# Performance work log

Hardware: AMD Instinct MI355X
Metric: run time of the kernel (lower is better)

## Reference

```python
import jax, jax.numpy as jnp
import numpy as np

DIM = 1536; NH = 12; HD = 128; C2 = HD // 2          # rope half-dim = 64
F, H, W = 1, 30, 52
FRAME = H * W                                         # 1560 tokens/frame
SINK_FRAMES = 1; LOCAL_ATTN = 6
SINK = SINK_FRAMES * FRAME                            # 1560
MAX_ATTN = LOCAL_ATTN * 1560                          # 9360
CACHE = 9360                                          # kv cache length
GLOBAL_END = 9360; LOCAL_END_CACHE = 9360             # cache state before step
SPLITS = (C2 - 2 * (C2 // 3), C2 // 3, C2 // 3)       # (22, 21, 21)
EPS = 1e-6


def setup_inputs() -> dict:
    key = jax.random.key(0)
    ks = jax.random.split(key, 12)
    s = F * H * W
    rn = lambda k, sh, sc=1.0: jax.random.normal(k, sh, jnp.float32) * sc
    x = rn(ks[0], (1, s, DIM))
    Wq = rn(ks[1], (DIM, DIM), 0.02); Wk = rn(ks[2], (DIM, DIM), 0.02)
    Wv = rn(ks[3], (DIM, DIM), 0.02); Wo = rn(ks[4], (DIM, DIM), 0.02)
    zb = jnp.zeros((DIM,), jnp.float32)
    angles = jax.random.uniform(ks[5], (1024, C2), jnp.float32) * (2.0 * np.pi)
    freqs_cos = jnp.cos(angles); freqs_sin = jnp.sin(angles)
    cache_k = rn(ks[6], (1, CACHE, NH, HD)); cache_v = rn(ks[7], (1, CACHE, NH, HD))
    return dict(x=x, Wq=Wq, bq=zb, Wk=Wk, bk=zb, Wv=Wv, bv=zb, Wo=Wo, bo=zb,
                nq_w=jnp.ones((DIM,), jnp.float32), nk_w=jnp.ones((DIM,), jnp.float32),
                cache_k=cache_k, cache_v=cache_v,
                freqs_cos=freqs_cos, freqs_sin=freqs_sin,
                seq_lens=jnp.array([s], jnp.int32),
                grid_sizes=jnp.array([[F, H, W]], jnp.int32),
                current_start=GLOBAL_END)


def _rmsnorm(x, w):
    return x * jax.lax.rsqrt(jnp.mean(x * x, -1, keepdims=True) + EPS) * w


def _grid_table(table, start_frame):
    """table [1024, C2] -> per-token rope factors [S, 1, C2] over the (F,H,W) grid."""
    s0, s1, s2 = SPLITS
    tf, th, tw = table[:, :s0], table[:, s0:s0 + s1], table[:, s0 + s1:]
    fp = jnp.broadcast_to(tf[start_frame:start_frame + F][:, None, None, :], (F, H, W, s0))
    hp = jnp.broadcast_to(th[:H][None, :, None, :], (F, H, W, s1))
    wp = jnp.broadcast_to(tw[:W][None, None, :, :], (F, H, W, s2))
    return jnp.concatenate([fp, hp, wp], -1).reshape(F * H * W, 1, C2)


def _rope(x, cos, sin):
    # x: [b, s, n, d]; cos/sin: [s, 1, C2] (complex multiply in real arithmetic)
    b, s, n, d = x.shape
    xp = x.reshape(b, s, n, d // 2, 2)
    xr, xi = xp[..., 0], xp[..., 1]
    c, sn = cos[None], sin[None]                      # [1, s, 1, C2]
    out_r = xr * c - xi * sn
    out_i = xr * sn + xi * c
    return jnp.stack([out_r, out_i], -1).reshape(b, s, n, d)


def reference(x, Wq, bq, Wk, bk, Wv, bv, Wo, bo, nq_w, nk_w,
              cache_k, cache_v, freqs_cos, freqs_sin,
              seq_lens, grid_sizes, current_start):
    b, s = x.shape[:2]
    q = _rmsnorm(x @ Wq.T + bq, nq_w).reshape(b, s, NH, HD)
    k = _rmsnorm(x @ Wk.T + bk, nk_w).reshape(b, s, NH, HD)
    v = (x @ Wv.T + bv).reshape(b, s, NH, HD)

    start_frame = int(current_start) // FRAME
    cos = _grid_table(freqs_cos, start_frame)
    sin = _grid_table(freqs_sin, start_frame)
    rq = _rope(q, cos, sin)
    rk = _rope(k, cos, sin)

    # --- static cache bookkeeping (roll_and_insert path; all Python ints) ---
    num_new = s
    current_end = int(current_start) + num_new
    num_evicted = num_new + LOCAL_END_CACHE - CACHE           # 1560
    num_rolled = LOCAL_END_CACHE - num_evicted - SINK         # 6240
    local_end = LOCAL_END_CACHE + current_end - GLOBAL_END - num_evicted  # 9360
    local_start = local_end - num_new                         # 7800 == SINK + num_rolled
    temp_k = jnp.concatenate(
        [cache_k[:, :SINK], cache_k[:, SINK + num_evicted:SINK + num_evicted + num_rolled], rk], axis=1)
    temp_v = jnp.concatenate(
        [cache_v[:, :SINK], cache_v[:, SINK + num_evicted:SINK + num_evicted + num_rolled], v], axis=1)

    # --- sink + sliding-window attention ---
    local_budget = MAX_ATTN - SINK
    win_start = max(SINK, local_end - local_budget)
    k_cat = jnp.concatenate([temp_k[:, :SINK], temp_k[:, win_start:local_end]], axis=1)
    v_cat = jnp.concatenate([temp_v[:, :SINK], temp_v[:, win_start:local_end]], axis=1)

    logits = jnp.einsum('bqhd,bkhd->bhqk', rq, k_cat) * (HD ** -0.5)
    probs = jax.nn.softmax(logits, axis=-1)
    out = jnp.einsum('bhqk,bkhd->bqhd', probs, v_cat)
    y = out.reshape(b, s, DIM) @ Wo.T + bo
    return y
```

## Files before the change

### kernel.cpp

```cpp
#include <hip/hip_runtime.h>
#include <hip/hip_bf16.h>

typedef __bf16 bf16;
typedef __bf16 bf16x2 __attribute__((ext_vector_type(2)));
typedef __bf16 bf16x4 __attribute__((ext_vector_type(4)));
typedef __bf16 bf16x8 __attribute__((ext_vector_type(8)));
typedef float f32x4 __attribute__((ext_vector_type(4)));

#define DIM 1536
#define NH 12
#define HD 128
#define SEQ 1560
#define KV 9360
#define KVP 9408
#define SINK 1560
#define NEWBASE 7800
#define QSCALE 0.08838834764831845f
#define NSPLIT 3
#define CHUNK 3136
#define NT 49
#define QBLK 128
#define NQT 13

__device__ __forceinline__ void gl_lds16(const void* g, void* l) {
  __builtin_amdgcn_global_load_lds(
      (const __attribute__((address_space(1))) unsigned int*)g,
      (__attribute__((address_space(3))) unsigned int*)l, 16, 0, 0);
}

__global__ __launch_bounds__(256) void castk(const float* __restrict__ src,
                                             bf16* __restrict__ dst, int n) {
  int i = (blockIdx.x * 256 + threadIdx.x) * 8;
  if (i < n) {
    float4 a = *(const float4*)(src + i);
    float4 b = *(const float4*)(src + i + 4);
    bf16x8 o;
    o[0] = (bf16)a.x; o[1] = (bf16)a.y; o[2] = (bf16)a.z; o[3] = (bf16)a.w;
    o[4] = (bf16)b.x; o[5] = (bf16)b.y; o[6] = (bf16)b.z; o[7] = (bf16)b.w;
    *(bf16x8*)(dst + i) = o;
  }
}

struct GemmBatch {
  const bf16* B[3];
  const float* bias[3];
  float* C[3];
};

#define BM 128
#define BN 128
#define BK 32

__global__ __launch_bounds__(256, 2) void gemm_bt(const bf16* __restrict__ A,
                                                  GemmBatch gb, int M) {
  const bf16* Bw = gb.B[blockIdx.z];
  const float* bias = gb.bias[blockIdx.z];
  float* C = gb.C[blockIdx.z];
  int bm = blockIdx.x * BM;
  int bn = blockIdx.y * BN;

  __shared__ bf16 Alds[2][BM][BK];
  __shared__ bf16 Blds[2][BN][BK];

  int t = threadIdx.x;
  int lane = t & 63;
  int wave = t >> 6;
  int wr = wave >> 1, wc = wave & 1;
  int fr = lane & 15;
  int fo = (lane >> 4) * 8;

  f32x4 acc[4][4] = {};

  const int NK = DIM / BK;
  int colA = (lane & 3) * 8;
  int lrow = lane >> 2;

#define STAGEG(buf, k0)                                                     \
  {                                                                         \
    _Pragma("unroll") for (int p = 0; p < 2; ++p) {                         \
      int rbase = wave * 16 + p * 64;                                       \
      int ga = bm + rbase + lrow;                                           \
      if (ga > M - 1) ga = M - 1;                                           \
      gl_lds16(A + (size_t)ga * DIM + (k0) + colA, &Alds[buf][rbase][0]);   \
      int gbv = bn + rbase + lrow;                                          \
      gl_lds16(Bw + (size_t)gbv * DIM + (k0) + colA, &Blds[buf][rbase][0]); \
    }                                                                       \
  }

  STAGEG(0, 0);
  int cur = 0;
  for (int ks = 0; ks < NK; ++ks) {
    __syncthreads();
    if (ks + 1 < NK) STAGEG(cur ^ 1, (ks + 1) * BK);
    bf16x8 af[4], bfv[4];
#pragma unroll
    for (int i = 0; i < 4; ++i)
      af[i] = *(const bf16x8*)&Alds[cur][wr * 64 + i * 16 + fr][fo];
#pragma unroll
    for (int j = 0; j < 4; ++j)
      bfv[j] = *(const bf16x8*)&Blds[cur][wc * 64 + j * 16 + fr][fo];
#pragma unroll
    for (int i = 0; i < 4; ++i)
#pragma unroll
      for (int j = 0; j < 4; ++j)
        acc[i][j] = __builtin_amdgcn_mfma_f32_16x16x32_bf16(af[i], bfv[j],
                                                            acc[i][j], 0, 0, 0);
    cur ^= 1;
  }
#undef STAGEG

  int g4 = (lane >> 4) * 4;
#pragma unroll
  for (int i = 0; i < 4; ++i) {
    int mbase = bm + wr * 64 + i * 16 + g4;
#pragma unroll
    for (int j = 0; j < 4; ++j) {
      int col = bn + wc * 64 + j * 16 + fr;
      float bv = bias[col];
#pragma unroll
      for (int r = 0; r < 4; ++r) {
        int m = mbase + r;
        if (m < M) C[(size_t)m * DIM + col] = acc[i][j][r] + bv;
      }
    }
  }
}

__global__ __launch_bounds__(256) void norm_rope(
    const float* __restrict__ qraw, const float* __restrict__ kraw,
    const float* __restrict__ nqw, const float* __restrict__ nkw,
    const float* __restrict__ fcos, const float* __restrict__ fsin,
    bf16* __restrict__ Qh, bf16* __restrict__ Kcat) {
  int tok = blockIdx.x;
  int tid = threadIdx.x;
  const float* qr = qraw + (size_t)tok * DIM;
  const float* kr = kraw + (size_t)tok * DIM;
  float sq = 0.f, sk = 0.f;
  for (int c = tid; c < DIM; c += 256) {
    float a = qr[c];
    sq += a * a;
    float b = kr[c];
    sk += b * b;
  }
#pragma unroll
  for (int off = 32; off; off >>= 1) {
    sq += __shfl_down(sq, off);
    sk += __shfl_down(sk, off);
  }
  __shared__ float red[2][4];
  int w = tid >> 6;
  if ((tid & 63) == 0) {
    red[0][w] = sq;
    red[1][w] = sk;
  }
  __syncthreads();
  sq = red[0][0] + red[0][1] + red[0][2] + red[0][3];
  sk = red[1][0] + red[1][1] + red[1][2] + red[1][3];
  float rsq = rsqrtf(sq * (1.0f / DIM) + 1e-6f);
  float rsk = rsqrtf(sk * (1.0f / DIM) + 1e-6f);

  int hrow = tok / 52, wrow = tok % 52;
  for (int p = tid; p < NH * 64; p += 256) {
    int n = p >> 6, i = p & 63;
    int trow = (i < 22) ? 6 : (i < 43 ? hrow : wrow);
    float cs = fcos[trow * 64 + i];
    float sn = fsin[trow * 64 + i];
    int c = n * HD + 2 * i;
    float xr = qr[c] * rsq * nqw[c];
    float xi = qr[c + 1] * rsq * nqw[c + 1];
    bf16x2 qo;
    qo[0] = (bf16)((xr * cs - xi * sn) * QSCALE);
    qo[1] = (bf16)((xr * sn + xi * cs) * QSCALE);
    *(bf16x2*)(Qh + ((size_t)n * SEQ + tok) * HD + 2 * i) = qo;
    float yr = kr[c] * rsk * nkw[c];
    float yi = kr[c + 1] * rsk * nkw[c + 1];
    bf16x2 ko;
    ko[0] = (bf16)(yr * cs - yi * sn);
    ko[1] = (bf16)(yr * sn + yi * cs);
    *(bf16x2*)(Kcat + ((size_t)n * KVP + NEWBASE + tok) * HD + 2 * i) = ko;
  }
}

__global__ __launch_bounds__(256) void build_kcat(const float* __restrict__ cache_k,
                                                  bf16* __restrict__ Kcat) {
  int j = blockIdx.x;
  int src = j < SINK ? j : j + SINK;
  const float* sp = cache_k + (size_t)src * DIM;
  for (int c4 = threadIdx.x; c4 < DIM / 4; c4 += 256) {
    float4 v = *(const float4*)(sp + c4 * 4);
    int c = c4 * 4;
    int n = c >> 7, d = c & 127;
    bf16x4 o;
    o[0] = (bf16)v.x; o[1] = (bf16)v.y; o[2] = (bf16)v.z; o[3] = (bf16)v.w;
    *(bf16x4*)(Kcat + ((size_t)n * KVP + j) * HD + d) = o;
  }
}

__global__ __launch_bounds__(256) void build_vt(const float* __restrict__ cache_v,
                                                const float* __restrict__ vraw,
                                                bf16* __restrict__ Vt) {
  int h = blockIdx.y;
  int j0 = blockIdx.x * 64;
  __shared__ bf16 T[128][72];
  int tid = threadIdx.x;
  for (int idx = tid; idx < 64 * 32; idx += 256) {
    int jl = idx >> 5, s = idx & 31;
    int j = j0 + jl;
    if (j >= KV) continue;
    const float* sp;
    if (j < NEWBASE) {
      int srcj = j < SINK ? j : j + SINK;
      sp = cache_v + (size_t)srcj * DIM + h * HD;
    } else {
      sp = vraw + (size_t)(j - NEWBASE) * DIM + h * HD;
    }
    float4 v = *(const float4*)(sp + s * 4);
    T[s * 4 + 0][jl] = (bf16)v.x;
    T[s * 4 + 1][jl] = (bf16)v.y;
    T[s * 4 + 2][jl] = (bf16)v.z;
    T[s * 4 + 3][jl] = (bf16)v.w;
  }
  __syncthreads();
  for (int idx = tid; idx < 128 * 16; idx += 256) {
    int d = idx >> 4, g = idx & 15;
    int j = j0 + g * 4;
    if (j + 4 > KV) continue;
    bf16x4 o;
    o[0] = T[d][4 * g];
    o[1] = T[d][4 * g + 1];
    o[2] = T[d][4 * g + 2];
    o[3] = T[d][4 * g + 3];
    *(bf16x4*)(Vt + ((size_t)h * HD + d) * KVP + j) = o;
  }
}

__global__ __launch_bounds__(256, 2) void attn_split(const bf16* __restrict__ Qh,
                                                     const bf16* __restrict__ Kcat,
                                                     const bf16* __restrict__ Vt,
                                                     float* __restrict__ Opart,
                                                     float* __restrict__ MLpart) {
  int orig = blockIdx.x;
  int xcd = orig & 7, jj = orig >> 3;
  int wgid = (xcd < 4 ? xcd * 59 : 236 + (xcd - 4) * 58) + jj;
  int qt = wgid % NQT;
  int h = (wgid / NQT) % NH;
  int sp = wgid / (NQT * NH);
  int q0 = qt * QBLK;
  int c0 = sp * CHUNK;

  int t = threadIdx.x, lane = t & 63, w = t >> 6;
  int g = lane >> 4, fr = lane & 15, s3 = fr & 7;

  __shared__ bf16 Klds[2][64][128];
  __shared__ bf16 Vlds[2][128][64];
  __shared__ bf16 Plds[4][2][16][64];

  bf16x8 qf[2][4];
#pragma unroll
  for (int s = 0; s < 2; ++s) {
    int qrow = q0 + w * 32 + s * 16 + fr;
    int qcl = qrow < SEQ ? qrow : SEQ - 1;
    const bf16* Qp = Qh + ((size_t)h * SEQ + qcl) * HD + g * 8;
#pragma unroll
    for (int fk = 0; fk < 4; ++fk) qf[s][fk] = *(const bf16x8*)(Qp + 32 * fk);
  }

  int kadd[4], vadd[4];
#pragma unroll
  for (int p = 0; p < 4; ++p) {
    int m = (4 * w + p) * 64 + lane;
    int rK = m >> 4, cK = m & 15;
    kadd[p] = rK * HD + (cK ^ (rK & 7)) * 8;
    int dV = m >> 3, cV = m & 7;
    vadd[p] = dV * KVP + (cV ^ (dV & 7)) * 8;
  }
  char* Kbase = (char*)&Klds[0][0][0];
  char* Vbase = (char*)&Vlds[0][0][0];

  int koffr[4], voffc[2], poffc[2], pwb[4];
#pragma unroll
  for (int fk = 0; fk < 4; ++fk) koffr[fk] = fr * 256 + (((g + 4 * fk) ^ s3) * 16);
#pragma unroll
  for (int c = 0; c < 2; ++c) {
    voffc[c] = fr * 128 + (((g + 4 * c) ^ s3) * 16);
    poffc[c] = fr * 128 + (((4 * c + g) ^ s3) * 16);
  }
#pragma unroll
  for (int fj = 0; fj < 4; ++fj)
    pwb[fj] = fr * 128 + (((2 * fj + (g >> 1)) ^ s3) * 16) + (g & 1) * 8;
  char* PldsB0 = (char*)&Plds[w][0][0][0];
  char* PldsB1 = (char*)&Plds[w][1][0][0];

  const bf16* Khp = Kcat + (size_t)h * KVP * HD;
  const bf16* Vhp = Vt + (size_t)h * HD * KVP;

  f32x4 oacc[2][8] = {};
  float m_q[2] = {-1e30f, -1e30f};
  float l_q[2] = {0.f, 0.f};

#define STAGE(buf, j0)                                                   \
  {                                                                      \
    const bf16* Ks = Khp + (size_t)(j0)*HD;                              \
    const bf16* Vs = Vhp + (j0);                                         \
    _Pragma("unroll") for (int p = 0; p < 4; ++p)                        \
        gl_lds16(Ks + kadd[p], Kbase + (buf)*16384 + w * 4096 + p * 1024); \
    _Pragma("unroll") for (int p = 0; p < 4; ++p)                        \
        gl_lds16(Vs + vadd[p], Vbase + (buf)*16384 + w * 4096 + p * 1024); \
  }

  STAGE(0, c0);
  __syncthreads();
  int cur = 0;

  for (int ti = 0; ti < NT; ++ti) {
    int j0 = c0 + ti * 64;
    if (ti + 1 < NT) STAGE(cur ^ 1, j0 + 64);

    const char* Kc = Kbase + cur * 16384;
    const char* Vc = Vbase + cur * 16384;

    f32x4 sacc[2][4] = {};
    __builtin_amdgcn_s_setprio(1);
#pragma unroll
    for (int fj = 0; fj < 4; ++fj)
#pragma unroll
      for (int fk = 0; fk < 4; ++fk) {
        bf16x8 kf = *(const bf16x8*)(Kc + fj * 4096 + koffr[fk]);
        sacc[0][fj] = __builtin_amdgcn_mfma_f32_16x16x32_bf16(kf, qf[0][fk], sacc[0][fj], 0, 0, 0);
        sacc[1][fj] = __builtin_amdgcn_mfma_f32_16x16x32_bf16(kf, qf[1][fk], sacc[1][fj], 0, 0, 0);
      }
    __builtin_amdgcn_s_setprio(0);

    if (j0 + 64 > KV) {
#pragma unroll
      for (int fj = 0; fj < 4; ++fj)
#pragma unroll
        for (int r = 0; r < 4; ++r)
          if (j0 + 16 * fj + 4 * g + r >= KV) {
            sacc[0][fj][r] = -1e30f;
            sacc[1][fj][r] = -1e30f;
          }
    }

#pragma unroll
    for (int s = 0; s < 2; ++s) {
      float mx = sacc[s][0][0];
#pragma unroll
      for (int fj = 0; fj < 4; ++fj)
#pragma unroll
        for (int r = 0; r < 4; ++r)
          if (fj | r) mx = fmaxf(mx, sacc[s][fj][r]);
      mx = fmaxf(mx, __shfl_xor(mx, 16));
      mx = fmaxf(mx, __shfl_xor(mx, 32));
      float mnew = fmaxf(m_q[s], mx);
      float corr = __expf(m_q[s] - mnew);
      m_q[s] = mnew;
      float sum = 0.f;
      bf16x4 pw[4];
#pragma unroll
      for (int fj = 0; fj < 4; ++fj)
#pragma unroll
        for (int r = 0; r < 4; ++r) {
          float e = __expf(sacc[s][fj][r] - mnew);
          pw[fj][r] = (bf16)e;
          sum += e;
        }
      sum += __shfl_xor(sum, 16);
      sum += __shfl_xor(sum, 32);
      l_q[s] = l_q[s] * corr + sum;

      float corr_r[4];
#pragma unroll
      for (int r = 0; r < 4; ++r) corr_r[r] = __shfl(corr, 4 * g + r);
#pragma unroll
      for (int fd = 0; fd < 8; ++fd)
#pragma unroll
        for (int r = 0; r < 4; ++r) oacc[s][fd][r] *= corr_r[r];

      char* PB = s ? PldsB1 : PldsB0;
#pragma unroll
      for (int fj = 0; fj < 4; ++fj) *(bf16x4*)(PB + pwb[fj]) = pw[fj];
    }

    bf16x8 pa[2][2];
#pragma unroll
    for (int c = 0; c < 2; ++c) {
      pa[0][c] = *(const bf16x8*)(PldsB0 + poffc[c]);
      pa[1][c] = *(const bf16x8*)(PldsB1 + poffc[c]);
    }
    __builtin_amdgcn_s_setprio(1);
#pragma unroll
    for (int fd = 0; fd < 8; ++fd) {
      bf16x8 v0 = *(const bf16x8*)(Vc + fd * 2048 + voffc[0]);
      bf16x8 v1 = *(const bf16x8*)(Vc + fd * 2048 + voffc[1]);
      oacc[0][fd] = __builtin_amdgcn_mfma_f32_16x16x32_bf16(pa[0][0], v0, oacc[0][fd], 0, 0, 0);
      oacc[0][fd] = __builtin_amdgcn_mfma_f32_16x16x32_bf16(pa[0][1], v1, oacc[0][fd], 0, 0, 0);
      oacc[1][fd] = __builtin_amdgcn_mfma_f32_16x16x32_bf16(pa[1][0], v0, oacc[1][fd], 0, 0, 0);
      oacc[1][fd] = __builtin_amdgcn_mfma_f32_16x16x32_bf16(pa[1][1], v1, oacc[1][fd], 0, 0, 0);
    }
    __builtin_amdgcn_s_setprio(0);

    __syncthreads();
    cur ^= 1;
  }
#undef STAGE

  float* Oh = Opart + ((size_t)sp * NH + h) * SEQ * HD;
  float* MLh = MLpart + ((size_t)sp * NH + h) * SEQ * 2;
#pragma unroll
  for (int s = 0; s < 2; ++s) {
#pragma unroll
    for (int r = 0; r < 4; ++r) {
      int q = q0 + w * 32 + s * 16 + 4 * g + r;
      if (q >= SEQ) continue;
#pragma unroll
      for (int fd = 0; fd < 8; ++fd)
        Oh[(size_t)q * HD + fr + 16 * fd] = oacc[s][fd][r];
    }
  }
  if (lane < 16) {
#pragma unroll
    for (int s = 0; s < 2; ++s) {
      int q = q0 + w * 32 + s * 16 + lane;
      if (q < SEQ) {
        MLh[q * 2 + 0] = m_q[s];
        MLh[q * 2 + 1] = l_q[s];
      }
    }
  }
}

__global__ __launch_bounds__(256) void attn_merge(const float* __restrict__ Opart,
                                                  const float* __restrict__ MLpart,
                                                  bf16* __restrict__ Aout) {
  int idx = blockIdx.x * 2 + (threadIdx.x >> 7);
  if (idx >= NH * SEQ) return;
  int d = threadIdx.x & 127;
  int h = idx / SEQ, q = idx % SEQ;
  float m[NSPLIT];
  float M = -1e30f;
#pragma unroll
  for (int s = 0; s < NSPLIT; ++s) {
    m[s] = MLpart[(((size_t)s * NH + h) * SEQ + q) * 2];
    M = fmaxf(M, m[s]);
  }
  float L = 0.f, o = 0.f;
#pragma unroll
  for (int s = 0; s < NSPLIT; ++s) {
    float wgt = __expf(m[s] - M);
    L += MLpart[(((size_t)s * NH + h) * SEQ + q) * 2 + 1] * wgt;
    o += Opart[((((size_t)s * NH + h) * SEQ + q)) * HD + d] * wgt;
  }
  Aout[(size_t)q * DIM + h * HD + d] = (bf16)(o / L);
}

extern "C" void kernel_launch(void* const* d_in, const int* in_sizes, int n_in,
                              void* d_out, int out_size, void* d_ws, size_t ws_size,
                              hipStream_t stream) {
  const float* x = (const float*)d_in[0];
  const float* Wq = (const float*)d_in[1];
  const float* bq = (const float*)d_in[2];
  const float* Wk = (const float*)d_in[3];
  const float* bk = (const float*)d_in[4];
  const float* Wv = (const float*)d_in[5];
  const float* bv = (const float*)d_in[6];
  const float* Wo = (const float*)d_in[7];
  const float* bo = (const float*)d_in[8];
  const float* nqw = (const float*)d_in[9];
  const float* nkw = (const float*)d_in[10];
  const float* cache_k = (const float*)d_in[11];
  const float* cache_v = (const float*)d_in[12];
  const float* fcos = (const float*)d_in[13];
  const float* fsin = (const float*)d_in[14];
  float* out = (float*)d_out;

  char* ws = (char*)d_ws;
  size_t off = 0;
  auto alloc = [&](size_t bytes) {
    char* p = ws + off;
    off += (bytes + 255) & ~(size_t)255;
    return p;
  };
  const int XN = SEQ * DIM;
  const int WN = DIM * DIM;
  bf16* xb = (bf16*)alloc((size_t)XN * 2);
  bf16* Wqb = (bf16*)alloc((size_t)WN * 2);
  bf16* Wkb = (bf16*)alloc((size_t)WN * 2);
  bf16* Wvb = (bf16*)alloc((size_t)WN * 2);
  bf16* Wob = (bf16*)alloc((size_t)WN * 2);
  float* qraw = (float*)alloc((size_t)XN * 4);
  float* kraw = (float*)alloc((size_t)XN * 4);
  float* vraw = (float*)alloc((size_t)XN * 4);
  bf16* QhB = (bf16*)alloc((size_t)NH * SEQ * HD * 2);
  bf16* Kcat = (bf16*)alloc((size_t)NH * KVP * HD * 2);
  bf16* Vt = (bf16*)alloc((size_t)NH * HD * KVP * 2);
  bf16* Aout = (bf16*)alloc((size_t)XN * 2);
  float* Opart = (float*)alloc((size_t)NSPLIT * NH * SEQ * HD * 4);
  float* MLpart = (float*)alloc((size_t)NSPLIT * NH * SEQ * 2 * 4);

  castk<<<(XN + 2047) / 2048, 256, 0, stream>>>(x, xb, XN);
  castk<<<(WN + 2047) / 2048, 256, 0, stream>>>(Wq, Wqb, WN);
  castk<<<(WN + 2047) / 2048, 256, 0, stream>>>(Wk, Wkb, WN);
  castk<<<(WN + 2047) / 2048, 256, 0, stream>>>(Wv, Wvb, WN);
  castk<<<(WN + 2047) / 2048, 256, 0, stream>>>(Wo, Wob, WN);

  GemmBatch gqkv;
  gqkv.B[0] = Wqb; gqkv.B[1] = Wkb; gqkv.B[2] = Wvb;
  gqkv.bias[0] = bq; gqkv.bias[1] = bk; gqkv.bias[2] = bv;
  gqkv.C[0] = qraw; gqkv.C[1] = kraw; gqkv.C[2] = vraw;
  gemm_bt<<<dim3(13, 12, 3), 256, 0, stream>>>(xb, gqkv, SEQ);

  norm_rope<<<SEQ, 256, 0, stream>>>(qraw, kraw, nqw, nkw, fcos, fsin, QhB, Kcat);
  build_kcat<<<NEWBASE, 256, 0, stream>>>(cache_k, Kcat);
  build_vt<<<dim3(147, NH), 256, 0, stream>>>(cache_v, vraw, Vt);

  attn_split<<<dim3(NQT * NH * NSPLIT), 256, 0, stream>>>(QhB, Kcat, Vt, Opart, MLpart);
  attn_merge<<<(NH * SEQ + 1) / 2, 256, 0, stream>>>(Opart, MLpart, Aout);

  GemmBatch gout;
  gout.B[0] = Wob; gout.B[1] = Wob; gout.B[2] = Wob;
  gout.bias[0] = bo; gout.bias[1] = bo; gout.bias[2] = bo;
  gout.C[0] = out; gout.C[1] = out; gout.C[2] = out;
  gemm_bt<<<dim3(13, 12, 1), 256, 0, stream>>>(Aout, gout, SEQ);
}
```

Before: 305.9 us.

## Raise attention occupancy with single-buffered LDS, more KV splits, and lazy rescaling

The attention kernel now stages K/V through registers into a single LDS buffer instead of double-buffered direct global-to-LDS loads. This halves shared memory so three workgroups fit per CU, and the KV dimension is split six ways instead of three. Softmax uses exp2 with log2(e) folded into the Q scale, and the running max and accumulator rescale only when the max grows by more than 8. The qkv scratch buffers alias the Opart buffer to save workspace. The cost is more merge work, an extra register round-trip for loads, and reduced load/compute overlap.

```diff
diff --git a/kernel.cpp b/kernel.cpp
--- a/kernel.cpp
+++ b/kernel.cpp
@@ -15,10 +15,9 @@
 #define KVP 9408
 #define SINK 1560
 #define NEWBASE 7800
-#define QSCALE 0.08838834764831845f
-#define NSPLIT 3
-#define CHUNK 3136
-#define NT 49
+#define QSCALE_L2E (0.08838834764831845f * 1.4426950408889634f)
+#define NSPLIT 6
+#define CHUNK 1600
 #define QBLK 128
 #define NQT 13
 
@@ -26,6 +25,13 @@
   __builtin_amdgcn_global_load_lds(
       (const __attribute__((address_space(1))) unsigned int*)g,
       (__attribute__((address_space(3))) unsigned int*)l, 16, 0, 0);
+}
+
+__device__ __forceinline__ f32x4 vmax4(f32x4 a, f32x4 b) {
+  f32x4 r;
+  r[0] = fmaxf(a[0], b[0]); r[1] = fmaxf(a[1], b[1]);
+  r[2] = fmaxf(a[2], b[2]); r[3] = fmaxf(a[3], b[3]);
+  return r;
 }
 
 __global__ __launch_bounds__(256) void castk(const float* __restrict__ src,
@@ -169,8 +175,8 @@
     float xr = qr[c] * rsq * nqw[c];
     float xi = qr[c + 1] * rsq * nqw[c + 1];
     bf16x2 qo;
-    qo[0] = (bf16)((xr * cs - xi * sn) * QSCALE);
-    qo[1] = (bf16)((xr * sn + xi * cs) * QSCALE);
+    qo[0] = (bf16)((xr * cs - xi * sn) * QSCALE_L2E);
+    qo[1] = (bf16)((xr * sn + xi * cs) * QSCALE_L2E);
     *(bf16x2*)(Qh + ((size_t)n * SEQ + tok) * HD + 2 * i) = qo;
     float yr = kr[c] * rsk * nkw[c];
     float yi = kr[c + 1] * rsk * nkw[c + 1];
@@ -234,26 +240,28 @@
   }
 }
 
-__global__ __launch_bounds__(256, 2) void attn_split(const bf16* __restrict__ Qh,
+__global__ __launch_bounds__(256, 3) void attn_split(const bf16* __restrict__ Qh,
                                                      const bf16* __restrict__ Kcat,
-                                                     const bf16* __restrict__ Vt,
+                                                     const bf16* __restrict__ Vtg,
                                                      float* __restrict__ Opart,
                                                      float* __restrict__ MLpart) {
   int orig = blockIdx.x;
-  int xcd = orig & 7, jj = orig >> 3;
-  int wgid = (xcd < 4 ? xcd * 59 : 236 + (xcd - 4) * 58) + jj;
+  int wgid = (orig & 7) * 117 + (orig >> 3);
   int qt = wgid % NQT;
-  int h = (wgid / NQT) % NH;
-  int sp = wgid / (NQT * NH);
+  int rest = wgid / NQT;
+  int h = rest % NH;
+  int sp = rest / NH;
   int q0 = qt * QBLK;
   int c0 = sp * CHUNK;
+  int cEnd = c0 + CHUNK < KVP ? c0 + CHUNK : KVP;
+  int nt = (cEnd - c0) >> 6;
 
   int t = threadIdx.x, lane = t & 63, w = t >> 6;
   int g = lane >> 4, fr = lane & 15, s3 = fr & 7;
 
-  __shared__ bf16 Klds[2][64][128];
-  __shared__ bf16 Vlds[2][128][64];
-  __shared__ bf16 Plds[4][2][16][64];
+  __shared__ __align__(16) bf16 Klds[64 * 128];
+  __shared__ __align__(16) bf16 Vlds[128 * 64];
+  __shared__ __align__(16) bf16 Plds[4][2][1024];
 
   bf16x8 qf[2][4];
 #pragma unroll
@@ -265,17 +273,17 @@
     for (int fk = 0; fk < 4; ++fk) qf[s][fk] = *(const bf16x8*)(Qp + 32 * fk);
   }
 
-  int kadd[4], vadd[4];
+  int kgo[4], vgo[4], kwo[4], vwo[4];
 #pragma unroll
   for (int p = 0; p < 4; ++p) {
     int m = (4 * w + p) * 64 + lane;
     int rK = m >> 4, cK = m & 15;
-    kadd[p] = rK * HD + (cK ^ (rK & 7)) * 8;
+    kgo[p] = rK * HD + cK * 8;
+    kwo[p] = rK * 256 + ((cK ^ (rK & 7)) * 16);
     int dV = m >> 3, cV = m & 7;
-    vadd[p] = dV * KVP + (cV ^ (dV & 7)) * 8;
-  }
-  char* Kbase = (char*)&Klds[0][0][0];
-  char* Vbase = (char*)&Vlds[0][0][0];
+    vgo[p] = dV * KVP + cV * 8;
+    vwo[p] = dV * 128 + ((cV ^ (dV & 7)) * 16);
+  }
 
   int koffr[4], voffc[2], poffc[2], pwb[4];
 #pragma unroll
@@ -288,36 +296,35 @@
 #pragma unroll
   for (int fj = 0; fj < 4; ++fj)
     pwb[fj] = fr * 128 + (((2 * fj + (g >> 1)) ^ s3) * 16) + (g & 1) * 8;
-  char* PldsB0 = (char*)&Plds[w][0][0][0];
-  char* PldsB1 = (char*)&Plds[w][1][0][0];
 
   const bf16* Khp = Kcat + (size_t)h * KVP * HD;
-  const bf16* Vhp = Vt + (size_t)h * HD * KVP;
+  const bf16* Vhp = Vtg + (size_t)h * HD * KVP;
+
+  int4 kreg[4], vreg[4];
+#define GLOAD(j)                                         \
+  {                                                      \
+    const bf16* Kt = Khp + (size_t)(j)*HD;               \
+    const bf16* Vp = Vhp + (j);                          \
+    _Pragma("unroll") for (int p = 0; p < 4; ++p) {      \
+      kreg[p] = *(const int4*)(Kt + kgo[p]);             \
+      vreg[p] = *(const int4*)(Vp + vgo[p]);             \
+    }                                                    \
+  }
 
   f32x4 oacc[2][8] = {};
-  float m_q[2] = {-1e30f, -1e30f};
+  float m_q[2] = {-1e38f, -1e38f};
   float l_q[2] = {0.f, 0.f};
 
-#define STAGE(buf, j0)                                                   \
-  {                                                                      \
-    const bf16* Ks = Khp + (size_t)(j0)*HD;                              \
-    const bf16* Vs = Vhp + (j0);                                         \
-    _Pragma("unroll") for (int p = 0; p < 4; ++p)                        \
-        gl_lds16(Ks + kadd[p], Kbase + (buf)*16384 + w * 4096 + p * 1024); \
-    _Pragma("unroll") for (int p = 0; p < 4; ++p)                        \
-        gl_lds16(Vs + vadd[p], Vbase + (buf)*16384 + w * 4096 + p * 1024); \
-  }
-
-  STAGE(0, c0);
-  __syncthreads();
-  int cur = 0;
-
-  for (int ti = 0; ti < NT; ++ti) {
+  GLOAD(c0);
+  for (int ti = 0; ti < nt; ++ti) {
     int j0 = c0 + ti * 64;
-    if (ti + 1 < NT) STAGE(cur ^ 1, j0 + 64);
-
-    const char* Kc = Kbase + cur * 16384;
-    const char* Vc = Vbase + cur * 16384;
+#pragma unroll
+    for (int p = 0; p < 4; ++p) {
+      *(int4*)((char*)Klds + kwo[p]) = kreg[p];
+      *(int4*)((char*)Vlds + vwo[p]) = vreg[p];
+    }
+    __syncthreads();
+    if (ti + 1 < nt) GLOAD(j0 + 64);
 
     f32x4 sacc[2][4] = {};
     __builtin_amdgcn_s_setprio(1);
@@ -325,7 +332,7 @@
     for (int fj = 0; fj < 4; ++fj)
 #pragma unroll
       for (int fk = 0; fk < 4; ++fk) {
-        bf16x8 kf = *(const bf16x8*)(Kc + fj * 4096 + koffr[fk]);
+        bf16x8 kf = *(const bf16x8*)((const char*)Klds + fj * 4096 + koffr[fk]);
         sacc[0][fj] = __builtin_amdgcn_mfma_f32_16x16x32_bf16(kf, qf[0][fk], sacc[0][fj], 0, 0, 0);
         sacc[1][fj] = __builtin_amdgcn_mfma_f32_16x16x32_bf16(kf, qf[1][fk], sacc[1][fj], 0, 0, 0);
       }
@@ -337,62 +344,70 @@
 #pragma unroll
         for (int r = 0; r < 4; ++r)
           if (j0 + 16 * fj + 4 * g + r >= KV) {
-            sacc[0][fj][r] = -1e30f;
-            sacc[1][fj][r] = -1e30f;
+            sacc[0][fj][r] = -1e38f;
+            sacc[1][fj][r] = -1e38f;
           }
     }
 
+    float mx[2];
 #pragma unroll
     for (int s = 0; s < 2; ++s) {
-      float mx = sacc[s][0][0];
-#pragma unroll
-      for (int fj = 0; fj < 4; ++fj)
-#pragma unroll
-        for (int r = 0; r < 4; ++r)
-          if (fj | r) mx = fmaxf(mx, sacc[s][fj][r]);
-      mx = fmaxf(mx, __shfl_xor(mx, 16));
-      mx = fmaxf(mx, __shfl_xor(mx, 32));
-      float mnew = fmaxf(m_q[s], mx);
-      float corr = __expf(m_q[s] - mnew);
-      m_q[s] = mnew;
-      float sum = 0.f;
+      f32x4 t4 = vmax4(vmax4(sacc[s][0], sacc[s][1]), vmax4(sacc[s][2], sacc[s][3]));
+      float m0 = fmaxf(fmaxf(t4[0], t4[1]), fmaxf(t4[2], t4[3]));
+      m0 = fmaxf(m0, __shfl_xor(m0, 16));
+      mx[s] = fmaxf(m0, __shfl_xor(m0, 32));
+    }
+    if (__any(fmaxf(mx[0] - m_q[0], mx[1] - m_q[1]) > 8.f)) {
+#pragma unroll
+      for (int s = 0; s < 2; ++s) {
+        float mnew = fmaxf(m_q[s], mx[s]);
+        float corr = exp2f(m_q[s] - mnew);
+        m_q[s] = mnew;
+        l_q[s] *= corr;
+        float corr_r[4];
+#pragma unroll
+        for (int r = 0; r < 4; ++r) corr_r[r] = __shfl(corr, 4 * g + r);
+#pragma unroll
+        for (int fd = 0; fd < 8; ++fd)
+#pragma unroll
+          for (int r = 0; r < 4; ++r) oacc[s][fd][r] *= corr_r[r];
+      }
+    }
+#pragma unroll
+    for (int s = 0; s < 2; ++s) {
+      f32x4 sum4 = {0.f, 0.f, 0.f, 0.f};
       bf16x4 pw[4];
 #pragma unroll
-      for (int fj = 0; fj < 4; ++fj)
+      for (int fj = 0; fj < 4; ++fj) {
 #pragma unroll
         for (int r = 0; r < 4; ++r) {
-          float e = __expf(sacc[s][fj][r] - mnew);
+          float e = exp2f(sacc[s][fj][r] - m_q[s]);
           pw[fj][r] = (bf16)e;
-          sum += e;
+          sum4[r] += e;
         }
+      }
+      float sum = (sum4[0] + sum4[1]) + (sum4[2] + sum4[3]);
       sum += __shfl_xor(sum, 16);
       sum += __shfl_xor(sum, 32);
-      l_q[s] = l_q[s] * corr + sum;
-
-      float corr_r[4];
-#pragma unroll
-      for (int r = 0; r < 4; ++r) corr_r[r] = __shfl(corr, 4 * g + r);
-#pragma unroll
-      for (int fd = 0; fd < 8; ++fd)
-#pragma unroll
-        for (int r = 0; r < 4; ++r) oacc[s][fd][r] *= corr_r[r];
-
-      char* PB = s ? PldsB1 : PldsB0;
+      l_q[s] += sum;
+      char* PB = (char*)&Plds[w][s][0];
 #pragma unroll
       for (int fj = 0; fj < 4; ++fj) *(bf16x4*)(PB + pwb[fj]) = pw[fj];
     }
 
     bf16x8 pa[2][2];
 #pragma unroll
-    for (int c = 0; c < 2; ++c) {
-      pa[0][c] = *(const bf16x8*)(PldsB0 + poffc[c]);
-      pa[1][c] = *(const bf16x8*)(PldsB1 + poffc[c]);
-    }
+    for (int s = 0; s < 2; ++s) {
+      const char* PB = (const char*)&Plds[w][s][0];
+      pa[s][0] = *(const bf16x8*)(PB + poffc[0]);
+      pa[s][1] = *(const bf16x8*)(PB + poffc[1]);
+    }
+
     __builtin_amdgcn_s_setprio(1);
 #pragma unroll
     for (int fd = 0; fd < 8; ++fd) {
-      bf16x8 v0 = *(const bf16x8*)(Vc + fd * 2048 + voffc[0]);
-      bf16x8 v1 = *(const bf16x8*)(Vc + fd * 2048 + voffc[1]);
+      bf16x8 v0 = *(const bf16x8*)((const char*)Vlds + fd * 2048 + voffc[0]);
+      bf16x8 v1 = *(const bf16x8*)((const char*)Vlds + fd * 2048 + voffc[1]);
       oacc[0][fd] = __builtin_amdgcn_mfma_f32_16x16x32_bf16(pa[0][0], v0, oacc[0][fd], 0, 0, 0);
       oacc[0][fd] = __builtin_amdgcn_mfma_f32_16x16x32_bf16(pa[0][1], v1, oacc[0][fd], 0, 0, 0);
       oacc[1][fd] = __builtin_amdgcn_mfma_f32_16x16x32_bf16(pa[1][0], v0, oacc[1][fd], 0, 0, 0);
@@ -401,9 +416,8 @@
     __builtin_amdgcn_s_setprio(0);
 
     __syncthreads();
-    cur ^= 1;
-  }
-#undef STAGE
+  }
+#undef GLOAD
 
   float* Oh = Opart + ((size_t)sp * NH + h) * SEQ * HD;
   float* MLh = MLpart + ((size_t)sp * NH + h) * SEQ * 2;
@@ -438,7 +452,7 @@
   int d = threadIdx.x & 127;
   int h = idx / SEQ, q = idx % SEQ;
   float m[NSPLIT];
-  float M = -1e30f;
+  float M = -1e38f;
 #pragma unroll
   for (int s = 0; s < NSPLIT; ++s) {
     m[s] = MLpart[(((size_t)s * NH + h) * SEQ + q) * 2];
@@ -447,7 +461,7 @@
   float L = 0.f, o = 0.f;
 #pragma unroll
   for (int s = 0; s < NSPLIT; ++s) {
-    float wgt = __expf(m[s] - M);
+    float wgt = exp2f(m[s] - M);
     L += MLpart[(((size_t)s * NH + h) * SEQ + q) * 2 + 1] * wgt;
     o += Opart[((((size_t)s * NH + h) * SEQ + q)) * HD + d] * wgt;
   }
@@ -488,15 +502,15 @@
   bf16* Wkb = (bf16*)alloc((size_t)WN * 2);
   bf16* Wvb = (bf16*)alloc((size_t)WN * 2);
   bf16* Wob = (bf16*)alloc((size_t)WN * 2);
-  float* qraw = (float*)alloc((size_t)XN * 4);
-  float* kraw = (float*)alloc((size_t)XN * 4);
-  float* vraw = (float*)alloc((size_t)XN * 4);
   bf16* QhB = (bf16*)alloc((size_t)NH * SEQ * HD * 2);
   bf16* Kcat = (bf16*)alloc((size_t)NH * KVP * HD * 2);
   bf16* Vt = (bf16*)alloc((size_t)NH * HD * KVP * 2);
   bf16* Aout = (bf16*)alloc((size_t)XN * 2);
+  float* MLpart = (float*)alloc((size_t)NSPLIT * NH * SEQ * 2 * 4);
   float* Opart = (float*)alloc((size_t)NSPLIT * NH * SEQ * HD * 4);
-  float* MLpart = (float*)alloc((size_t)NSPLIT * NH * SEQ * 2 * 4);
+  float* qraw = Opart;
+  float* kraw = qraw + XN;
+  float* vraw = kraw + XN;
 
   castk<<<(XN + 2047) / 2048, 256, 0, stream>>>(x, xb, XN);
   castk<<<(WN + 2047) / 2048, 256, 0, stream>>>(Wq, Wqb, WN);
```

Result: slower. 559.4 us (+82.9%).

## Use exp2 softmax with lazy rescale, batch weight casts, alias raw QKV buffers

Applied to the files above, without the earlier changes.

Folds log2(e) into the Q scale so the attention softmax can use exp2 directly. The online-softmax rescale of the output accumulators now runs only when some row's max rises by more than a threshold, which skips most per-tile correction multiplies. The four weight-cast launches are merged into one batched launch, and the raw QKV projection buffers now reuse the Opart workspace to cut the memory footprint. The lazy rescale lets exponent arguments exceed zero by a bounded amount, which slightly changes numerical behaviour.

```diff
diff --git a/kernel.cpp b/kernel.cpp
--- a/kernel.cpp
+++ b/kernel.cpp
@@ -15,7 +15,7 @@
 #define KVP 9408
 #define SINK 1560
 #define NEWBASE 7800
-#define QSCALE 0.08838834764831845f
+#define QSCALE_L2E (0.08838834764831845f * 1.4426950408889634f)
 #define NSPLIT 3
 #define CHUNK 3136
 #define NT 49
@@ -28,8 +28,33 @@
       (__attribute__((address_space(3))) unsigned int*)l, 16, 0, 0);
 }
 
+__device__ __forceinline__ f32x4 vmax4(f32x4 a, f32x4 b) {
+  f32x4 r;
+  r[0] = fmaxf(a[0], b[0]); r[1] = fmaxf(a[1], b[1]);
+  r[2] = fmaxf(a[2], b[2]); r[3] = fmaxf(a[3], b[3]);
+  return r;
+}
+
 __global__ __launch_bounds__(256) void castk(const float* __restrict__ src,
                                              bf16* __restrict__ dst, int n) {
+  int i = (blockIdx.x * 256 + threadIdx.x) * 8;
+  if (i < n) {
+    float4 a = *(const float4*)(src + i);
+    float4 b = *(const float4*)(src + i + 4);
+    bf16x8 o;
+    o[0] = (bf16)a.x; o[1] = (bf16)a.y; o[2] = (bf16)a.z; o[3] = (bf16)a.w;
+    o[4] = (bf16)b.x; o[5] = (bf16)b.y; o[6] = (bf16)b.z; o[7] = (bf16)b.w;
+    *(bf16x8*)(dst + i) = o;
+  }
+}
+
+struct CastBatch {
+  const float* src[4];
+  bf16* dst[4];
+};
+__global__ __launch_bounds__(256) void castw(CastBatch cb, int n) {
+  const float* src = cb.src[blockIdx.y];
+  bf16* dst = cb.dst[blockIdx.y];
   int i = (blockIdx.x * 256 + threadIdx.x) * 8;
   if (i < n) {
     float4 a = *(const float4*)(src + i);
@@ -169,8 +194,8 @@
     float xr = qr[c] * rsq * nqw[c];
     float xi = qr[c + 1] * rsq * nqw[c + 1];
     bf16x2 qo;
-    qo[0] = (bf16)((xr * cs - xi * sn) * QSCALE);
-    qo[1] = (bf16)((xr * sn + xi * cs) * QSCALE);
+    qo[0] = (bf16)((xr * cs - xi * sn) * QSCALE_L2E);
+    qo[1] = (bf16)((xr * sn + xi * cs) * QSCALE_L2E);
     *(bf16x2*)(Qh + ((size_t)n * SEQ + tok) * HD + 2 * i) = qo;
     float yr = kr[c] * rsk * nkw[c];
     float yi = kr[c + 1] * rsk * nkw[c + 1];
@@ -236,7 +261,7 @@
 
 __global__ __launch_bounds__(256, 2) void attn_split(const bf16* __restrict__ Qh,
                                                      const bf16* __restrict__ Kcat,
-                                                     const bf16* __restrict__ Vt,
+                                                     const bf16* __restrict__ Vtg,
                                                      float* __restrict__ Opart,
                                                      float* __restrict__ MLpart) {
   int orig = blockIdx.x;
@@ -292,10 +317,10 @@
   char* PldsB1 = (char*)&Plds[w][1][0][0];
 
   const bf16* Khp = Kcat + (size_t)h * KVP * HD;
-  const bf16* Vhp = Vt + (size_t)h * HD * KVP;
+  const bf16* Vhp = Vtg + (size_t)h * HD * KVP;
 
   f32x4 oacc[2][8] = {};
-  float m_q[2] = {-1e30f, -1e30f};
+  float m_q[2] = {-1e38f, -1e38f};
   float l_q[2] = {0.f, 0.f};
 
 #define STAGE(buf, j0)                                                   \
@@ -337,46 +362,53 @@
 #pragma unroll
         for (int r = 0; r < 4; ++r)
           if (j0 + 16 * fj + 4 * g + r >= KV) {
-            sacc[0][fj][r] = -1e30f;
-            sacc[1][fj][r] = -1e30f;
+            sacc[0][fj][r] = -1e38f;
+            sacc[1][fj][r] = -1e38f;
           }
     }
 
+    float mx[2];
 #pragma unroll
     for (int s = 0; s < 2; ++s) {
-      float mx = sacc[s][0][0];
-#pragma unroll
-      for (int fj = 0; fj < 4; ++fj)
-#pragma unroll
-        for (int r = 0; r < 4; ++r)
-          if (fj | r) mx = fmaxf(mx, sacc[s][fj][r]);
-      mx = fmaxf(mx, __shfl_xor(mx, 16));
-      mx = fmaxf(mx, __shfl_xor(mx, 32));
-      float mnew = fmaxf(m_q[s], mx);
-      float corr = __expf(m_q[s] - mnew);
-      m_q[s] = mnew;
-      float sum = 0.f;
+      f32x4 t4 = vmax4(vmax4(sacc[s][0], sacc[s][1]), vmax4(sacc[s][2], sacc[s][3]));
+      float m0 = fmaxf(fmaxf(t4[0], t4[1]), fmaxf(t4[2], t4[3]));
+      m0 = fmaxf(m0, __shfl_xor(m0, 16));
+      mx[s] = fmaxf(m0, __shfl_xor(m0, 32));
+    }
+    if (__any(fmaxf(mx[0] - m_q[0], mx[1] - m_q[1]) > 8.f)) {
+#pragma unroll
+      for (int s = 0; s < 2; ++s) {
+        float mnew = fmaxf(m_q[s], mx[s]);
+        float corr = exp2f(m_q[s] - mnew);
+        m_q[s] = mnew;
+        l_q[s] *= corr;
+        float corr_r[4];
+#pragma unroll
+        for (int r = 0; r < 4; ++r) corr_r[r] = __shfl(corr, 4 * g + r);
+#pragma unroll
+        for (int fd = 0; fd < 8; ++fd)
+#pragma unroll
+          for (int r = 0; r < 4; ++r) oacc[s][fd][r] *= corr_r[r];
+      }
+    }
+
+#pragma unroll
+    for (int s = 0; s < 2; ++s) {
+      f32x4 sum4 = {0.f, 0.f, 0.f, 0.f};
       bf16x4 pw[4];
 #pragma unroll
-      for (int fj = 0; fj < 4; ++fj)
+      for (int fj = 0; fj < 4; ++fj) {
 #pragma unroll
         for (int r = 0; r < 4; ++r) {
-          float e = __expf(sacc[s][fj][r] - mnew);
+          float e = exp2f(sacc[s][fj][r] - m_q[s]);
           pw[fj][r] = (bf16)e;
-          sum += e;
+          sum4[r] += e;
         }
+      }
+      float sum = (sum4[0] + sum4[1]) + (sum4[2] + sum4[3]);
       sum += __shfl_xor(sum, 16);
       sum += __shfl_xor(sum, 32);
-      l_q[s] = l_q[s] * corr + sum;
-
-      float corr_r[4];
-#pragma unroll
-      for (int r = 0; r < 4; ++r) corr_r[r] = __shfl(corr, 4 * g + r);
-#pragma unroll
-      for (int fd = 0; fd < 8; ++fd)
-#pragma unroll
-        for (int r = 0; r < 4; ++r) oacc[s][fd][r] *= corr_r[r];
-
+      l_q[s] += sum;
       char* PB = s ? PldsB1 : PldsB0;
 #pragma unroll
       for (int fj = 0; fj < 4; ++fj) *(bf16x4*)(PB + pwb[fj]) = pw[fj];
@@ -438,7 +470,7 @@
   int d = threadIdx.x & 127;
   int h = idx / SEQ, q = idx % SEQ;
   float m[NSPLIT];
-  float M = -1e30f;
+  float M = -1e38f;
 #pragma unroll
   for (int s = 0; s < NSPLIT; ++s) {
     m[s] = MLpart[(((size_t)s * NH + h) * SEQ + q) * 2];
@@ -447,7 +479,7 @@
   float L = 0.f, o = 0.f;
 #pragma unroll
   for (int s = 0; s < NSPLIT; ++s) {
-    float wgt = __expf(m[s] - M);
+    float wgt = exp2f(m[s] - M);
     L += MLpart[(((size_t)s * NH + h) * SEQ + q) * 2 + 1] * wgt;
     o += Opart[((((size_t)s * NH + h) * SEQ + q)) * HD + d] * wgt;
   }
@@ -488,21 +520,21 @@
   bf16* Wkb = (bf16*)alloc((size_t)WN * 2);
   bf16* Wvb = (bf16*)alloc((size_t)WN * 2);
   bf16* Wob = (bf16*)alloc((size_t)WN * 2);
-  float* qraw = (float*)alloc((size_t)XN * 4);
-  float* kraw = (float*)alloc((size_t)XN * 4);
-  float* vraw = (float*)alloc((size_t)XN * 4);
   bf16* QhB = (bf16*)alloc((size_t)NH * SEQ * HD * 2);
   bf16* Kcat = (bf16*)alloc((size_t)NH * KVP * HD * 2);
   bf16* Vt = (bf16*)alloc((size_t)NH * HD * KVP * 2);
   bf16* Aout = (bf16*)alloc((size_t)XN * 2);
+  float* MLpart = (float*)alloc((size_t)NSPLIT * NH * SEQ * 2 * 4);
   float* Opart = (float*)alloc((size_t)NSPLIT * NH * SEQ * HD * 4);
-  float* MLpart = (float*)alloc((size_t)NSPLIT * NH * SEQ * 2 * 4);
+  float* qraw = Opart;
+  float* kraw = qraw + XN;
+  float* vraw = kraw + XN;
 
   castk<<<(XN + 2047) / 2048, 256, 0, stream>>>(x, xb, XN);
-  castk<<<(WN + 2047) / 2048, 256, 0, stream>>>(Wq, Wqb, WN);
-  castk<<<(WN + 2047) / 2048, 256, 0, stream>>>(Wk, Wkb, WN);
-  castk<<<(WN + 2047) / 2048, 256, 0, stream>>>(Wv, Wvb, WN);
-  castk<<<(WN + 2047) / 2048, 256, 0, stream>>>(Wo, Wob, WN);
+  CastBatch cb;
+  cb.src[0] = Wq; cb.src[1] = Wk; cb.src[2] = Wv; cb.src[3] = Wo;
+  cb.dst[0] = Wqb; cb.dst[1] = Wkb; cb.dst[2] = Wvb; cb.dst[3] = Wob;
+  castw<<<dim3((WN + 2047) / 2048, 4), 256, 0, stream>>>(cb, WN);
 
   GemmBatch gqkv;
   gqkv.B[0] = Wqb; gqkv.B[1] = Wkb; gqkv.B[2] = Wvb;
```

After: 304.6 us. About the same (-0.4%).
